# Kernel optimization log

Hardware: AMD Instinct MI355X
Metric: run time of the kernel (lower is better)

Reference implementation:

```python
import jax, jax.numpy as jnp
import numpy as np

NUM_GROUPS = 4
DIVERSITY_STRENGTH = -0.5   # module stores -diversity_strength
DIVERSITY_DISCOUNT = 0.5
CAND_MULT = 1
N_GRAM = 2


def setup_inputs() -> dict:
    key = jax.random.key(0)
    k1, k2, k3, k5, k6 = jax.random.split(key, 5)
    bsz, beam, vocab, T = 64, 8, 50257, 128
    return {
        "lprobs": jax.random.normal(k1, (bsz, beam, vocab), jnp.float32),
        "scores": jax.random.normal(k2, (bsz, beam, T), jnp.float32),
        "group_overlap": jax.random.uniform(k3, (bsz, NUM_GROUPS, NUM_GROUPS), jnp.float32),
        "original_batch_idxs": jnp.arange(bsz, dtype=jnp.int32),
        "last_n_gram_indices": jax.random.randint(k5, (bsz, beam, N_GRAM - 1), 0, vocab, jnp.int32),
        "mask_last_n_gram_indices": jax.random.randint(k6, (bsz, beam, N_GRAM), 0, 2, jnp.int32),
        "step": 5,
    }


def reference(lprobs, scores, group_overlap, original_batch_idxs,
              last_n_gram_indices, mask_last_n_gram_indices, step):
    bsz, beam, vocab = lprobs.shape
    G = NUM_GROUPS
    mb = beam // G  # mini beam size
    k = CAND_MULT * mb
    batch_ar = jnp.arange(bsz)[:, None]

    scores_G, beams_G, idx_G = [], [], []
    for g in range(G):
        lp = lprobs[:, g::G, :]                       # [bsz, mb, vocab]
        sc = scores[:, g::G, step - 1]                # [bsz, mb]
        mk = mask_last_n_gram_indices[:, g::G, :]     # [bsz, mb, n_gram]
        if g > 0:
            # diversity penalty: scatter-add (1 + overlap) at previously picked tokens
            pen = 1.0 + group_overlap[original_batch_idxs, g, :g]          # [bsz, g]
            src = jnp.broadcast_to(pen[:, None, :], (bsz, mb, g)).reshape(bsz, -1)
            prev_idx = jnp.stack(idx_G, axis=-1).reshape(bsz, -1)          # [bsz, mb*g]
            div = jnp.zeros((bsz, vocab), lp.dtype).at[batch_ar, prev_idx].add(src)
            lp = lp + DIVERSITY_STRENGTH * div[:, None, :]
        # n-gram overlap mask: zero out beams whose mask rows are not all ones
        valid = (mk.sum(-1) == N_GRAM)                # [bsz, mb]
        lp = jnp.where(valid[:, :, None], lp, 0.0)
        # step > 0: add accumulated beam scores
        lp = lp + sc[:, :, None]
        flat = lp.reshape(bsz, -1)                    # [bsz, mb*vocab]
        top_idx = jax.lax.top_k(flat, k)[1]
        top_val = jnp.take_along_axis(flat, top_idx, axis=-1)
        beams_G.append((top_idx // vocab) * G + g)
        idx_G.append(top_idx % vocab)
        scores_G.append(top_val)

    scores_buf = jnp.stack(scores_G, axis=2).reshape(bsz, -1)   # [bsz, beam]
    indices_buf = jnp.stack(idx_G, axis=2).reshape(bsz, -1)
    beams_buf = jnp.stack(beams_G, axis=2).reshape(bsz, -1)

    # Hamming-cumulative overlap: [bsz, beam, n_gram] present n-grams, grouped
    present = jnp.concatenate(
        [last_n_gram_indices, indices_buf[:, :, None]], axis=-1
    ).reshape(bsz, mb, G, N_GRAM)
    eq = (present[:, :, None, :, :] == present[:, :, :, None, :])  # [bsz, mb, G, G, n]
    m = (mask_last_n_gram_indices != 0).reshape(bsz, mb, G, N_GRAM)
    om = m[:, :, None, :, :] & m[:, :, :, None, :]
    eq = jnp.where(om, eq, False)
    ov = (eq.sum(-1) == N_GRAM).astype(jnp.int32).sum(1)           # [bsz, G, G]

    new_group_overlap = (
        group_overlap.at[original_batch_idxs].add(ov.astype(group_overlap.dtype))
        * DIVERSITY_DISCOUNT
    )
    return scores_buf, indices_buf, beams_buf, new_group_overlap
```

## Files before the change

### kernel.cpp

```cpp
#include <hip/hip_runtime.h>
#include <math.h>

#define VOCAB 50257
#define BSZ   64
#define BEAM  8
#define NG    4
#define MB    2
#define KC    2
#define TLEN  128
#define NGRAM 2
#define SEG    64
#define SEGLEN 786
#define ROWS  (BSZ * BEAM)

__device__ __forceinline__ bool better(float v1, int i1, float v2, int i2) {
    return (v1 > v2) || (v1 == v2 && i1 < i2);
}

struct Top2 { float v1, v2; int i1, i2; };

__device__ __forceinline__ void t2_init(Top2& t) {
    t.v1 = -INFINITY; t.v2 = -INFINITY; t.i1 = 0x7FFFFFFF; t.i2 = 0x7FFFFFFF;
}

__device__ __forceinline__ void t2_push(Top2& t, float v, int i) {
    if (better(v, i, t.v2, t.i2)) {
        if (better(v, i, t.v1, t.i1)) { t.v2 = t.v1; t.i2 = t.i1; t.v1 = v; t.i1 = i; }
        else                          { t.v2 = v;    t.i2 = i; }
    }
}

__device__ __forceinline__ void t2_merge(Top2& a, const Top2& b) {
    if (better(b.v1, b.i1, a.v1, a.i1)) {
        float nv2; int ni2;
        if (better(a.v1, a.i1, b.v2, b.i2)) { nv2 = a.v1; ni2 = a.i1; }
        else                                { nv2 = b.v2; ni2 = b.i2; }
        a.v1 = b.v1; a.i1 = b.i1; a.v2 = nv2; a.i2 = ni2;
    } else {
        if (better(b.v1, b.i1, a.v2, a.i2)) { a.v2 = b.v1; a.i2 = b.i1; }
    }
}

__device__ __forceinline__ float max4(float4 v) {
    return fmaxf(fmaxf(v.x, v.y), fmaxf(v.z, v.w));
}

__global__ __launch_bounds__(256) void dbs_segmax(
    const float* __restrict__ lprobs,
    const int*   __restrict__ mask,
    float* __restrict__ wsmax,
    int*   __restrict__ wscnt)
{
    const int blk  = blockIdx.x;
    const int r    = blk >> 4;
    const int oct  = blk & 15;
    const int tid  = threadIdx.x;
    const int w    = tid >> 6, lane = tid & 63;

    if (oct == 0 && tid == 0) wscnt[r] = 0;
    if (mask[r * NGRAM] + mask[r * NGRAM + 1] != NGRAM) return;

    const int seg = oct * 4 + w;
    const size_t rowoff = (size_t)r * VOCAB;
    const float* row = lprobs + rowoff;
    const int start = seg * SEGLEN;
    const int end   = min(start + SEGLEN, VOCAB);

    float m = -INFINITY;
    const int mis = (int)((rowoff + start) & 3);
    const int pre = (4 - mis) & 3;
    if (lane < pre && start + lane < end) m = row[start + lane];
    const int vstart = start + pre;
    const int n4 = (end > vstart) ? ((end - vstart) >> 2) : 0;
    const float4* vrow = (const float4*)(row + vstart);

    float a0 = -INFINITY, a1 = -INFINITY, a2 = -INFINITY, a3 = -INFINITY;
    if (lane        < n4) a0 = max4(vrow[lane]);
    if (lane +  64  < n4) a1 = max4(vrow[lane + 64]);
    if (lane + 128  < n4) a2 = max4(vrow[lane + 128]);
    if (lane + 192  < n4) a3 = max4(vrow[lane + 192]);
    m = fmaxf(m, fmaxf(fmaxf(a0, a1), fmaxf(a2, a3)));
    const int tstart = vstart + 4 * n4;
    if (tstart + lane < end) m = fmaxf(m, row[tstart + lane]);

    #pragma unroll
    for (int off = 32; off > 0; off >>= 1) m = fmaxf(m, __shfl_xor(m, off));
    if (lane == 0) wsmax[r * SEG + seg] = m;
}

__device__ __forceinline__ void emit_cand(float v, int idx, int r, int cap,
                                          int* wscnt, float* wscv, int* wsci) {
    const int p = atomicAdd(&wscnt[r], 1);
    if (p < cap) {
        wscv[(size_t)r * cap + p] = v;
        wsci[(size_t)r * cap + p] = idx;
    }
}

__global__ __launch_bounds__(256) void dbs_compact(
    const float* __restrict__ lprobs,
    const int*   __restrict__ mask,
    const float* __restrict__ wsmax,
    int*   __restrict__ wscnt,
    float* __restrict__ wscv,
    int*   __restrict__ wsci,
    int cap)
{
    const int blk  = blockIdx.x;
    const int r    = blk >> 4;
    const int oct  = blk & 15;
    const int tid  = threadIdx.x;
    const int w    = tid >> 6, lane = tid & 63;

    if (mask[r * NGRAM] + mask[r * NGRAM + 1] != NGRAM) return;

    const float mym = wsmax[r * SEG + lane];
    int rank = 0;
    for (int i = 0; i < SEG; ++i) {
        const float om = __shfl(mym, i);
        rank += better(om, i, mym, lane) ? 1 : 0;
    }
    const unsigned long long bm = __ballot(rank == 7);
    const int src = __ffsll(bm) - 1;
    const float tau = __shfl(mym, src);

    const int seg = oct * 4 + w;
    const size_t rowoff = (size_t)r * VOCAB;
    const float* row = lprobs + rowoff;
    const int start = seg * SEGLEN;
    const int end   = min(start + SEGLEN, VOCAB);

    const int mis = (int)((rowoff + start) & 3);
    const int pre = (4 - mis) & 3;
    if (lane < pre && start + lane < end) {
        const float v = row[start + lane];
        if (v >= tau) emit_cand(v, start + lane, r, cap, wscnt, wscv, wsci);
    }
    const int vstart = start + pre;
    const int n4 = (end > vstart) ? ((end - vstart) >> 2) : 0;
    const float4* vrow = (const float4*)(row + vstart);

    #pragma unroll
    for (int u = 0; u < 4; ++u) {
        const int jj = lane + u * 64;
        if (jj < n4) {
            const float4 v = vrow[jj];
            if (max4(v) >= tau) {
                const int base = vstart + 4 * jj;
                if (v.x >= tau) emit_cand(v.x, base,     r, cap, wscnt, wscv, wsci);
                if (v.y >= tau) emit_cand(v.y, base + 1, r, cap, wscnt, wscv, wsci);
                if (v.z >= tau) emit_cand(v.z, base + 2, r, cap, wscnt, wscv, wsci);
                if (v.w >= tau) emit_cand(v.w, base + 3, r, cap, wscnt, wscv, wsci);
            }
        }
    }
    const int tstart = vstart + 4 * n4;
    if (tstart + lane < end) {
        const float v = row[tstart + lane];
        if (v >= tau) emit_cand(v, tstart + lane, r, cap, wscnt, wscv, wsci);
    }
}

__global__ __launch_bounds__(64) void dbs_final(
    const float* __restrict__ scores,
    const float* __restrict__ overlap,
    const int*   __restrict__ obi,
    const int*   __restrict__ lastn,
    const int*   __restrict__ mask,
    const int*   __restrict__ stepp,
    const int*   __restrict__ wscnt,
    const float* __restrict__ wscv,
    const int*   __restrict__ wsci,
    int cap,
    float*       __restrict__ out)
{
    const int b   = blockIdx.x;
    const int tid = threadIdx.x;
    const int step = stepp[0];
    const int ob   = obi[b];

    __shared__ float s_sc[BEAM];
    __shared__ int   s_valid[BEAM];
    __shared__ float s_pen[(NG-1)*KC];
    __shared__ int   s_penidx[(NG-1)*KC];
    __shared__ float s_selv[NG][KC];
    __shared__ int   s_seli[NG][KC];
    __shared__ int   s_selm[NG][KC];

    if (tid < BEAM) {
        const int* mk = mask + ((size_t)b * BEAM + tid) * NGRAM;
        s_valid[tid] = (mk[0] + mk[1]) == NGRAM;
        s_sc[tid]    = scores[((size_t)b * BEAM + tid) * TLEN + (step - 1)];
    }
    __syncthreads();

    for (int g = 0; g < NG; ++g) {
        if (tid == 0) {
            for (int j = 0; j < g; ++j) {
                const float pen = 1.0f + overlap[((size_t)ob * NG + g) * NG + j];
                s_penidx[j*KC + 0] = s_seli[j][0]; s_pen[j*KC + 0] = pen;
                s_penidx[j*KC + 1] = s_seli[j][1]; s_pen[j*KC + 1] = pen;
            }
        }
        __syncthreads();

        const int np = KC * g;
        Top2 t; t2_init(t);
        for (int m = 0; m < MB; ++m) {
            const int beam = m * NG + g;
            if (s_valid[beam]) {
                const int r = b * BEAM + beam;
                const int n = min(wscnt[r], cap);
                for (int c = tid; c < n; c += 64) {
                    const float v   = wscv[(size_t)r * cap + c];
                    const int   idx = wsci[(size_t)r * cap + c];
                    float dv = 0.0f;
                    #pragma unroll
                    for (int p = 0; p < (NG-1)*KC; ++p)
                        if (p < np && s_penidx[p] == idx) dv += s_pen[p];
                    t2_push(t, v - 0.5f * dv + s_sc[beam], m * VOCAB + idx);
                }
            } else if (tid < KC) {
                t2_push(t, s_sc[beam], m * VOCAB + tid);
            }
        }

        #pragma unroll
        for (int off = 32; off > 0; off >>= 1) {
            Top2 o;
            o.v1 = __shfl_down(t.v1, off); o.i1 = __shfl_down(t.i1, off);
            o.v2 = __shfl_down(t.v2, off); o.i2 = __shfl_down(t.i2, off);
            t2_merge(t, o);
        }
        if (tid == 0) {
            s_selv[g][0] = t.v1; s_seli[g][0] = t.i1 % VOCAB; s_selm[g][0] = t.i1 / VOCAB;
            s_selv[g][1] = t.v2; s_seli[g][1] = t.i2 % VOCAB; s_selm[g][1] = t.i2 / VOCAB;
        }
        __syncthreads();
    }

    if (tid < KC * NG) {
        const int i = tid;
        const int m = i / NG, g = i % NG;
        out[(size_t)b * BEAM + i]        = s_selv[g][m];
        out[512 + (size_t)b * BEAM + i]  = (float)s_seli[g][m];
        out[1024 + (size_t)b * BEAM + i] = (float)(s_selm[g][m] * NG + g);
    }
    if (tid >= 16 && tid < 16 + NG * NG) {
        const int q  = tid - 16;
        const int g1 = q / NG, g2 = q % NG;
        int ov = 0;
        for (int m = 0; m < MB; ++m) {
            const int i1 = m * NG + g1, i2 = m * NG + g2;
            const int p1a = lastn[(size_t)b * BEAM + i1];
            const int p2a = lastn[(size_t)b * BEAM + i2];
            const int p1b = s_seli[g1][m];
            const int p2b = s_seli[g2][m];
            const int* mk1 = mask + ((size_t)b * BEAM + i1) * NGRAM;
            const int* mk2 = mask + ((size_t)b * BEAM + i2) * NGRAM;
            const bool e0 = (p1a == p2a) && (mk1[0] != 0) && (mk2[0] != 0);
            const bool e1 = (p1b == p2b) && (mk1[1] != 0) && (mk2[1] != 0);
            ov += (e0 && e1) ? 1 : 0;
        }
        out[1536 + (size_t)ob * (NG * NG) + q] =
            (overlap[(size_t)ob * (NG * NG) + q] + (float)ov) * 0.5f;
    }
}

extern "C" void kernel_launch(void* const* d_in, const int* in_sizes, int n_in,
                              void* d_out, int out_size, void* d_ws, size_t ws_size,
                              hipStream_t stream) {
    const float* lprobs  = (const float*)d_in[0];
    const float* scores  = (const float*)d_in[1];
    const float* overlap = (const float*)d_in[2];
    const int*   obi     = (const int*)d_in[3];
    const int*   lastn   = (const int*)d_in[4];
    const int*   mask    = (const int*)d_in[5];
    const int*   stepp   = (const int*)d_in[6];
    float*       out     = (float*)d_out;

    float* wsmax = (float*)d_ws;
    int*   wscnt = (int*)((char*)d_ws + (size_t)ROWS * SEG * 4);
    const size_t fixed = (size_t)ROWS * SEG * 4 + ROWS * 4;
    size_t avail = (ws_size > fixed) ? (ws_size - fixed) : 0;
    int cap = (int)(avail / ((size_t)ROWS * 8));
    if (cap > 256) cap = 256;
    if (cap < 8)   cap = 8;
    float* wscv = (float*)((char*)d_ws + fixed);
    int*   wsci = (int*)((char*)d_ws + fixed + (size_t)ROWS * cap * 4);

    dbs_segmax <<<ROWS * 16, 256, 0, stream>>>(lprobs, mask, wsmax, wscnt);
    dbs_compact<<<ROWS * 16, 256, 0, stream>>>(lprobs, mask, wsmax, wscnt,
                                               wscv, wsci, cap);
    dbs_final  <<<BSZ, 64, 0, stream>>>(scores, overlap, obi, lastn, mask, stepp,
                                        wscnt, wscv, wsci, cap, out);
}
```

Baseline: 31.25 us.

## Fuse segment-max and candidate compaction into one per-row kernel

Merges the segment-max and compaction kernels into a single kernel with one 1024-thread block per row. The 64 segment maxima and the threshold now live in shared memory, and candidates are gathered with shared-memory atomics before being written out. This removes one kernel launch, the global workspace round trip for the maxima, and the global atomics. The row's second pass is more likely to be served from cache because the same block reads it shortly after the first. In exchange, parallelism drops to one block per row. The workspace is assumed to hold a fixed 1024-entry capacity per row, and the provided ws_size is no longer checked against that.

```diff
diff --git a/kernel.cpp b/kernel.cpp
--- a/kernel.cpp
+++ b/kernel.cpp
@@ -12,6 +12,7 @@
 #define SEG    64
 #define SEGLEN 786
 #define ROWS  (BSZ * BEAM)
+#define CAP   1024
 
 __device__ __forceinline__ bool better(float v1, int i1, float v2, int i2) {
     return (v1 > v2) || (v1 == v2 && i1 < i2);
@@ -45,119 +46,125 @@
     return fmaxf(fmaxf(v.x, v.y), fmaxf(v.z, v.w));
 }
 
-__global__ __launch_bounds__(256) void dbs_segmax(
+__global__ __launch_bounds__(1024) void dbs_candidates(
     const float* __restrict__ lprobs,
     const int*   __restrict__ mask,
-    float* __restrict__ wsmax,
-    int*   __restrict__ wscnt)
+    int*   __restrict__ wscnt,
+    float* __restrict__ wscv,
+    int*   __restrict__ wsci)
 {
-    const int blk  = blockIdx.x;
-    const int r    = blk >> 4;
-    const int oct  = blk & 15;
+    const int r    = blockIdx.x;
     const int tid  = threadIdx.x;
     const int w    = tid >> 6, lane = tid & 63;
 
-    if (oct == 0 && tid == 0) wscnt[r] = 0;
     if (mask[r * NGRAM] + mask[r * NGRAM + 1] != NGRAM) return;
 
-    const int seg = oct * 4 + w;
+    __shared__ float s_max[SEG];
+    __shared__ float s_tau;
+    __shared__ int   s_cnt;
+    __shared__ float s_cv[CAP];
+    __shared__ int   s_ci[CAP];
+
+    if (tid == 0) s_cnt = 0;
+
     const size_t rowoff = (size_t)r * VOCAB;
     const float* row = lprobs + rowoff;
-    const int start = seg * SEGLEN;
-    const int end   = min(start + SEGLEN, VOCAB);
-
-    float m = -INFINITY;
-    const int mis = (int)((rowoff + start) & 3);
-    const int pre = (4 - mis) & 3;
-    if (lane < pre && start + lane < end) m = row[start + lane];
-    const int vstart = start + pre;
-    const int n4 = (end > vstart) ? ((end - vstart) >> 2) : 0;
-    const float4* vrow = (const float4*)(row + vstart);
-
-    float a0 = -INFINITY, a1 = -INFINITY, a2 = -INFINITY, a3 = -INFINITY;
-    if (lane        < n4) a0 = max4(vrow[lane]);
-    if (lane +  64  < n4) a1 = max4(vrow[lane + 64]);
-    if (lane + 128  < n4) a2 = max4(vrow[lane + 128]);
-    if (lane + 192  < n4) a3 = max4(vrow[lane + 192]);
-    m = fmaxf(m, fmaxf(fmaxf(a0, a1), fmaxf(a2, a3)));
-    const int tstart = vstart + 4 * n4;
-    if (tstart + lane < end) m = fmaxf(m, row[tstart + lane]);
 
     #pragma unroll
-    for (int off = 32; off > 0; off >>= 1) m = fmaxf(m, __shfl_xor(m, off));
-    if (lane == 0) wsmax[r * SEG + seg] = m;
-}
-
-__device__ __forceinline__ void emit_cand(float v, int idx, int r, int cap,
-                                          int* wscnt, float* wscv, int* wsci) {
-    const int p = atomicAdd(&wscnt[r], 1);
-    if (p < cap) {
-        wscv[(size_t)r * cap + p] = v;
-        wsci[(size_t)r * cap + p] = idx;
-    }
-}
-
-__global__ __launch_bounds__(256) void dbs_compact(
-    const float* __restrict__ lprobs,
-    const int*   __restrict__ mask,
-    const float* __restrict__ wsmax,
-    int*   __restrict__ wscnt,
-    float* __restrict__ wscv,
-    int*   __restrict__ wsci,
-    int cap)
-{
-    const int blk  = blockIdx.x;
-    const int r    = blk >> 4;
-    const int oct  = blk & 15;
-    const int tid  = threadIdx.x;
-    const int w    = tid >> 6, lane = tid & 63;
-
-    if (mask[r * NGRAM] + mask[r * NGRAM + 1] != NGRAM) return;
-
-    const float mym = wsmax[r * SEG + lane];
-    int rank = 0;
-    for (int i = 0; i < SEG; ++i) {
-        const float om = __shfl(mym, i);
-        rank += better(om, i, mym, lane) ? 1 : 0;
-    }
-    const unsigned long long bm = __ballot(rank == 7);
-    const int src = __ffsll(bm) - 1;
-    const float tau = __shfl(mym, src);
-
-    const int seg = oct * 4 + w;
-    const size_t rowoff = (size_t)r * VOCAB;
-    const float* row = lprobs + rowoff;
-    const int start = seg * SEGLEN;
-    const int end   = min(start + SEGLEN, VOCAB);
-
-    const int mis = (int)((rowoff + start) & 3);
-    const int pre = (4 - mis) & 3;
-    if (lane < pre && start + lane < end) {
-        const float v = row[start + lane];
-        if (v >= tau) emit_cand(v, start + lane, r, cap, wscnt, wscv, wsci);
-    }
-    const int vstart = start + pre;
-    const int n4 = (end > vstart) ? ((end - vstart) >> 2) : 0;
-    const float4* vrow = (const float4*)(row + vstart);
+    for (int s = 0; s < 4; ++s) {
+        const int seg   = w * 4 + s;
+        const int start = seg * SEGLEN;
+        const int end   = min(start + SEGLEN, VOCAB);
+        const int mis   = (int)((rowoff + start) & 3);
+        const int pre   = (4 - mis) & 3;
+
+        float m = -INFINITY;
+        if (lane < pre && start + lane < end) m = row[start + lane];
+        const int vstart = start + pre;
+        const int n4 = (end > vstart) ? ((end - vstart) >> 2) : 0;
+        const float4* vrow = (const float4*)(row + vstart);
+
+        float a0 = -INFINITY, a1 = -INFINITY, a2 = -INFINITY, a3 = -INFINITY;
+        if (lane       < n4) a0 = max4(vrow[lane]);
+        if (lane +  64 < n4) a1 = max4(vrow[lane + 64]);
+        if (lane + 128 < n4) a2 = max4(vrow[lane + 128]);
+        if (lane + 192 < n4) a3 = max4(vrow[lane + 192]);
+        m = fmaxf(m, fmaxf(fmaxf(a0, a1), fmaxf(a2, a3)));
+        const int tstart = vstart + 4 * n4;
+        if (tstart + lane < end) m = fmaxf(m, row[tstart + lane]);
+
+        #pragma unroll
+        for (int off = 32; off > 0; off >>= 1) m = fmaxf(m, __shfl_xor(m, off));
+        if (lane == 0) s_max[seg] = m;
+    }
+    __syncthreads();
+
+    if (w == 0) {
+        const float mym = s_max[lane];
+        int rank = 0;
+        for (int i = 0; i < SEG; ++i) {
+            const float om = __shfl(mym, i);
+            rank += better(om, i, mym, lane) ? 1 : 0;
+        }
+        if (rank == 7) s_tau = mym;
+    }
+    __syncthreads();
+    const float tau = s_tau;
 
     #pragma unroll
-    for (int u = 0; u < 4; ++u) {
-        const int jj = lane + u * 64;
-        if (jj < n4) {
-            const float4 v = vrow[jj];
-            if (max4(v) >= tau) {
-                const int base = vstart + 4 * jj;
-                if (v.x >= tau) emit_cand(v.x, base,     r, cap, wscnt, wscv, wsci);
-                if (v.y >= tau) emit_cand(v.y, base + 1, r, cap, wscnt, wscv, wsci);
-                if (v.z >= tau) emit_cand(v.z, base + 2, r, cap, wscnt, wscv, wsci);
-                if (v.w >= tau) emit_cand(v.w, base + 3, r, cap, wscnt, wscv, wsci);
-            }
-        }
-    }
-    const int tstart = vstart + 4 * n4;
-    if (tstart + lane < end) {
-        const float v = row[tstart + lane];
-        if (v >= tau) emit_cand(v, tstart + lane, r, cap, wscnt, wscv, wsci);
+    for (int s = 0; s < 4; ++s) {
+        const int seg   = w * 4 + s;
+        const int start = seg * SEGLEN;
+        const int end   = min(start + SEGLEN, VOCAB);
+        const int mis   = (int)((rowoff + start) & 3);
+        const int pre   = (4 - mis) & 3;
+
+        if (lane < pre && start + lane < end) {
+            const float v = row[start + lane];
+            if (v >= tau) {
+                const int p = atomicAdd(&s_cnt, 1);
+                if (p < CAP) { s_cv[p] = v; s_ci[p] = start + lane; }
+            }
+        }
+        const int vstart = start + pre;
+        const int n4 = (end > vstart) ? ((end - vstart) >> 2) : 0;
+        const float4* vrow = (const float4*)(row + vstart);
+
+        #pragma unroll
+        for (int u = 0; u < 4; ++u) {
+            const int jj = lane + u * 64;
+            if (jj < n4) {
+                const float4 v = vrow[jj];
+                if (max4(v) >= tau) {
+                    const int base = vstart + 4 * jj;
+                    #pragma unroll
+                    for (int e = 0; e < 4; ++e) {
+                        const float ve = (e == 0) ? v.x : (e == 1) ? v.y
+                                       : (e == 2) ? v.z : v.w;
+                        if (ve >= tau) {
+                            const int p = atomicAdd(&s_cnt, 1);
+                            if (p < CAP) { s_cv[p] = ve; s_ci[p] = base + e; }
+                        }
+                    }
+                }
+            }
+        }
+        const int tstart = vstart + 4 * n4;
+        if (tstart + lane < end) {
+            const float v = row[tstart + lane];
+            if (v >= tau) {
+                const int p = atomicAdd(&s_cnt, 1);
+                if (p < CAP) { s_cv[p] = v; s_ci[p] = tstart + lane; }
+            }
+        }
+    }
+    __syncthreads();
+
+    const int cnt = min(s_cnt, CAP);
+    if (tid == 0) wscnt[r] = cnt;
+    for (int c = tid; c < cnt; c += 1024) {
+        wscv[(size_t)r * CAP + c] = s_cv[c];
+        wsci[(size_t)r * CAP + c] = s_ci[c];
     }
 }
 
@@ -171,7 +178,6 @@
     const int*   __restrict__ wscnt,
     const float* __restrict__ wscv,
     const int*   __restrict__ wsci,
-    int cap,
     float*       __restrict__ out)
 {
     const int b   = blockIdx.x;
@@ -210,10 +216,10 @@
             const int beam = m * NG + g;
             if (s_valid[beam]) {
                 const int r = b * BEAM + beam;
-                const int n = min(wscnt[r], cap);
+                const int n = wscnt[r];
                 for (int c = tid; c < n; c += 64) {
-                    const float v   = wscv[(size_t)r * cap + c];
-                    const int   idx = wsci[(size_t)r * cap + c];
+                    const float v   = wscv[(size_t)r * CAP + c];
+                    const int   idx = wsci[(size_t)r * CAP + c];
                     float dv = 0.0f;
                     #pragma unroll
                     for (int p = 0; p < (NG-1)*KC; ++p)
@@ -279,19 +285,11 @@
     const int*   stepp   = (const int*)d_in[6];
     float*       out     = (float*)d_out;
 
-    float* wsmax = (float*)d_ws;
-    int*   wscnt = (int*)((char*)d_ws + (size_t)ROWS * SEG * 4);
-    const size_t fixed = (size_t)ROWS * SEG * 4 + ROWS * 4;
-    size_t avail = (ws_size > fixed) ? (ws_size - fixed) : 0;
-    int cap = (int)(avail / ((size_t)ROWS * 8));
-    if (cap > 256) cap = 256;
-    if (cap < 8)   cap = 8;
-    float* wscv = (float*)((char*)d_ws + fixed);
-    int*   wsci = (int*)((char*)d_ws + fixed + (size_t)ROWS * cap * 4);
-
-    dbs_segmax <<<ROWS * 16, 256, 0, stream>>>(lprobs, mask, wsmax, wscnt);
-    dbs_compact<<<ROWS * 16, 256, 0, stream>>>(lprobs, mask, wsmax, wscnt,
-                                               wscv, wsci, cap);
-    dbs_final  <<<BSZ, 64, 0, stream>>>(scores, overlap, obi, lastn, mask, stepp,
-                                        wscnt, wscv, wsci, cap, out);
-}
+    int*   wscnt = (int*)d_ws;
+    float* wscv  = (float*)((char*)d_ws + ROWS * 4);
+    int*   wsci  = (int*)((char*)d_ws + ROWS * 4 + (size_t)ROWS * CAP * 4);
+
+    dbs_candidates<<<ROWS, 1024, 0, stream>>>(lprobs, mask, wscnt, wscv, wsci);
+    dbs_final     <<<BSZ, 64, 0, stream>>>(scores, overlap, obi, lastn, mask, stepp,
+                                           wscnt, wscv, wsci, out);
+}
```

Result: faster. 27.20 us (-13.0%).
